# Kernel optimization log

Measured on AMD Instinct MI355X. Metric: run time of the kernel, lower is better.

The kernel has to match this reference:

```python
import jax, jax.numpy as jnp
import numpy as np

S, B, D, H = 2048, 2, 1024, 16
DK = D // H  # 64

def setup_inputs() -> dict:
    key0 = jax.random.key(0)
    ks = jax.random.split(key0, 11)
    scale = 0.02
    inp = {
        'query': jax.random.normal(ks[0], (S, B, D), jnp.float32),
        'key':   jax.random.normal(ks[1], (S, B, D), jnp.float32),
        'value': jax.random.normal(ks[2], (S, B, D), jnp.float32),
        # nn.Linear weights stored torch-style [out_features, in_features]
        'Wq': jax.random.normal(ks[3], (H * DK, D), jnp.float32) * scale,
        'bq': jnp.zeros((H * DK,), jnp.float32),
        'Wk': jax.random.normal(ks[4], (H * DK, D), jnp.float32) * scale,
        'bk': jnp.zeros((H * DK,), jnp.float32),
        'Wv': jax.random.normal(ks[5], (H * DK, D), jnp.float32) * scale,
        'bv': jnp.zeros((H * DK,), jnp.float32),
        'Wo': jax.random.normal(ks[6], (D, D), jnp.float32) * scale,
        'bo': jnp.zeros((D,), jnp.float32),
    }
    return inp

def _proj(x, W, b):
    # x: [S,B,D] -> [S,B,H,DK]
    y = jnp.einsum('sbd,ed->sbe', x, W) + b
    return y.reshape(x.shape[0], x.shape[1], H, DK)

def reference(query, key, value, Wq, bq, Wk, bk, Wv, bv, Wo, bo):
    q = _proj(query, Wq, bq)   # [S,B,H,DK]
    k = _proj(key,   Wk, bk)
    v = _proj(value, Wv, bv)
    # NOTE: original forward never applies self.scale -> unscaled QK^T (faithful)
    scores = jnp.einsum('ibhd,jbhd->ijbh', q, k)      # [Sq,Sk,B,H]
    attn = jax.nn.softmax(scores, axis=1)             # softmax over key axis j
    x = jnp.einsum('ijbh,jbhd->ibhd', attn, v)        # [S,B,H,DK]
    x = x.reshape(q.shape[0], q.shape[1], H * DK)     # [S,B,D]
    out = jnp.einsum('sbd,ed->sbe', x, Wo) + bo       # [S,B,D]
    return out
```

## Files before the change

### kernel.cpp

```cpp
#include <hip/hip_runtime.h>
#include <stdint.h>

#define S_LEN  2048
#define BATCH  2
#define DMODEL 1024
#define NHEAD  16
#define DKH    64

typedef __attribute__((ext_vector_type(8))) __bf16 bf16x8;
typedef __attribute__((ext_vector_type(4))) float  f32x4;
typedef unsigned short u16;
typedef unsigned int   u32;

#if __has_builtin(__builtin_amdgcn_exp2f)
#define EXP2(x) __builtin_amdgcn_exp2f(x)
#else
#define EXP2(x) __expf(0.69314718055994531f * (x))
#endif

#define SWAP32(a, b) asm("v_permlane32_swap_b32 %0, %1" : "+v"(a), "+v"(b))
#define SWAP16(a, b) asm("v_permlane16_swap_b32 %0, %1" : "+v"(a), "+v"(b))

__device__ __forceinline__ u16 f2bf(float f) {
  union { float f; u32 u; } v; v.f = f;
  u32 r = v.u + 0x7fffu + ((v.u >> 16) & 1u);
  return (u16)(r >> 16);
}

__global__ void cvt3_kernel(const float4* __restrict__ a, const float4* __restrict__ b,
                            const float4* __restrict__ c,
                            ushort4* __restrict__ oa, ushort4* __restrict__ ob,
                            ushort4* __restrict__ oc, int n4) {
  int i = blockIdx.x * blockDim.x + threadIdx.x;
  if (i >= n4) return;
  const float4* src = (blockIdx.y == 0) ? a : (blockIdx.y == 1) ? b : c;
  ushort4*      dst = (blockIdx.y == 0) ? oa : (blockIdx.y == 1) ? ob : oc;
  float4 v = src[i];
  ushort4 o;
  o.x = f2bf(v.x); o.y = f2bf(v.y); o.z = f2bf(v.z); o.w = f2bf(v.w);
  dst[i] = o;
}

__global__ void cvt4_kernel(const float4* __restrict__ a, const float4* __restrict__ b,
                            const float4* __restrict__ c, const float4* __restrict__ d,
                            ushort4* __restrict__ oa, ushort4* __restrict__ ob,
                            ushort4* __restrict__ oc, ushort4* __restrict__ od, int n4) {
  int i = blockIdx.x * blockDim.x + threadIdx.x;
  if (i >= n4) return;
  const float4* src = (blockIdx.y == 0) ? a : (blockIdx.y == 1) ? b : (blockIdx.y == 2) ? c : d;
  ushort4*      dst = (blockIdx.y == 0) ? oa : (blockIdx.y == 1) ? ob : (blockIdx.y == 2) ? oc : od;
  float4 v = src[i];
  ushort4 o;
  o.x = f2bf(v.x); o.y = f2bf(v.y); o.z = f2bf(v.z); o.w = f2bf(v.w);
  dst[i] = o;
}

__global__ __launch_bounds__(256, 2)
void gemm_qkv(const u16* __restrict__ Abase, const u16* __restrict__ Wbase,
              const float* __restrict__ b0, const float* __restrict__ b1,
              const float* __restrict__ b2, u16* __restrict__ Obase) {
  __shared__ __align__(16) u16 As[128 * 32];
  __shared__ __align__(16) u16 Bs[128 * 32];

  const int z = blockIdx.z;
  const u16* A = Abase + (size_t)z * (S_LEN * BATCH * DMODEL);
  const u16* W = Wbase + (size_t)z * (DMODEL * DMODEL);
  const float* bias = (z == 0) ? b0 : (z == 1) ? b1 : b2;
  u16* O = Obase + (size_t)z * (S_LEN * BATCH * DMODEL);
  const float scl = (z == 0) ? 1.4426950408889634f : 1.0f;

  const int tid  = threadIdx.x;
  const int wave = tid >> 6, lane = tid & 63;
  const int quad = lane >> 4, lcol = lane & 15;
  const int m0 = blockIdx.y * 128, n0 = blockIdx.x * 128;
  const int wm = (wave >> 1) * 64, wn = (wave & 1) * 64;

  f32x4 acc[4][4] = {};

  for (int k0 = 0; k0 < DMODEL; k0 += 32) {
#pragma unroll
    for (int r = 0; r < 2; ++r) {
      int idx = r * 256 + tid;
      int row = idx >> 2, col = (idx & 3) * 8;
      const u16* gA = A + (size_t)(m0 + row) * DMODEL + k0 + col;
      const u16* gW = W + (size_t)(n0 + row) * DMODEL + k0 + col;
      u16* lA = As + (size_t)(r * 256 + (tid & 192)) * 8;
      u16* lB = Bs + (size_t)(r * 256 + (tid & 192)) * 8;
      __builtin_amdgcn_global_load_lds((const __attribute__((address_space(1))) void*)gA,
                                       (__attribute__((address_space(3))) void*)lA, 16, 0, 0);
      __builtin_amdgcn_global_load_lds((const __attribute__((address_space(1))) void*)gW,
                                       (__attribute__((address_space(3))) void*)lB, 16, 0, 0);
    }
    __syncthreads();

    const u16* aBase = As + (wm + lcol) * 32 + quad * 8;
    const u16* bBase = Bs + (wn + lcol) * 32 + quad * 8;
    bf16x8 af[4], bfr[4];
#pragma unroll
    for (int i = 0; i < 4; ++i) af[i]  = *(const bf16x8*)(aBase + i * 16 * 32);
#pragma unroll
    for (int j = 0; j < 4; ++j) bfr[j] = *(const bf16x8*)(bBase + j * 16 * 32);
#pragma unroll
    for (int i = 0; i < 4; ++i)
#pragma unroll
      for (int j = 0; j < 4; ++j)
        acc[i][j] = __builtin_amdgcn_mfma_f32_16x16x32_bf16(af[i], bfr[j], acc[i][j], 0, 0, 0);
    __syncthreads();
  }

#pragma unroll
  for (int i = 0; i < 4; ++i) {
#pragma unroll
    for (int j = 0; j < 4; ++j) {
      int n = n0 + wn + j * 16 + lcol;
      int h = n >> 6, dk = n & 63;
      float bv = bias[n];
#pragma unroll
      for (int r = 0; r < 4; ++r) {
        int m = m0 + wm + i * 16 + quad * 4 + r;
        int s = m >> 1, b = m & 1;
        O[((size_t)(b * NHEAD + h) * S_LEN + s) * DKH + dk] = f2bf((acc[i][j][r] + bv) * scl);
      }
    }
  }
}

__global__ __launch_bounds__(256, 2)
void gemm_o(const u16* __restrict__ A, const u16* __restrict__ W,
            const float* __restrict__ bias, float* __restrict__ O) {
  __shared__ __align__(16) u16 As[128 * 32];
  __shared__ __align__(16) u16 Bs[64 * 32];

  const int tid  = threadIdx.x;
  const int wave = tid >> 6, lane = tid & 63;
  const int quad = lane >> 4, lcol = lane & 15;
  const int m0 = blockIdx.y * 128, n0 = blockIdx.x * 64;
  const int wm = (wave >> 1) * 64, wn = (wave & 1) * 32;

  f32x4 acc[4][2] = {};

  for (int k0 = 0; k0 < DMODEL; k0 += 32) {
#pragma unroll
    for (int r = 0; r < 2; ++r) {
      int idx = r * 256 + tid;
      int row = idx >> 2, col = (idx & 3) * 8;
      const u16* gA = A + (size_t)(m0 + row) * DMODEL + k0 + col;
      u16* lA = As + (size_t)(r * 256 + (tid & 192)) * 8;
      __builtin_amdgcn_global_load_lds((const __attribute__((address_space(1))) void*)gA,
                                       (__attribute__((address_space(3))) void*)lA, 16, 0, 0);
    }
    {
      int row = tid >> 2, col = (tid & 3) * 8;
      const u16* gW = W + (size_t)(n0 + row) * DMODEL + k0 + col;
      u16* lB = Bs + (size_t)(tid & 192) * 8;
      __builtin_amdgcn_global_load_lds((const __attribute__((address_space(1))) void*)gW,
                                       (__attribute__((address_space(3))) void*)lB, 16, 0, 0);
    }
    __syncthreads();

    const u16* aBase = As + (wm + lcol) * 32 + quad * 8;
    const u16* bBase = Bs + (wn + lcol) * 32 + quad * 8;
    bf16x8 af[4], bfr[2];
#pragma unroll
    for (int i = 0; i < 4; ++i) af[i]  = *(const bf16x8*)(aBase + i * 16 * 32);
#pragma unroll
    for (int j = 0; j < 2; ++j) bfr[j] = *(const bf16x8*)(bBase + j * 16 * 32);
#pragma unroll
    for (int i = 0; i < 4; ++i)
#pragma unroll
      for (int j = 0; j < 2; ++j)
        acc[i][j] = __builtin_amdgcn_mfma_f32_16x16x32_bf16(af[i], bfr[j], acc[i][j], 0, 0, 0);
    __syncthreads();
  }

#pragma unroll
  for (int i = 0; i < 4; ++i) {
#pragma unroll
    for (int j = 0; j < 2; ++j) {
      int n = n0 + wn + j * 16 + lcol;
      float bv = bias[n];
#pragma unroll
      for (int r = 0; r < 4; ++r) {
        int m = m0 + wm + i * 16 + quad * 4 + r;
        O[(size_t)m * DMODEL + n] = acc[i][j][r] + bv;
      }
    }
  }
}

__global__ __launch_bounds__(512, 4)
void attn_kernel(const u16* __restrict__ Q, const u16* __restrict__ K,
                 const u16* __restrict__ V, u16* __restrict__ O) {
  __shared__ __align__(16) u16 smem[2 * 4608 + 2 * 4608];
  __shared__ float l_s2[4][32];
  u16* Ks  = smem;
  u16* Vts = smem + 2 * 4608;

  const int tid  = threadIdx.x;
  const int wave = tid >> 6, lane = tid & 63;
  const int quad = lane >> 4, lcol = lane & 15;
  const int h  = wave >> 2;
  const int qw = wave & 3;
  const int bh = blockIdx.y;
  const int q0 = blockIdx.x * 128;

  const size_t headOff = (size_t)bh * S_LEN * DKH;
  const u16* Qg = Q + headOff;
  const u16* Kg = K + headOff;
  const u16* Vg = V + headOff;

  bf16x8 qf[2][2];
#pragma unroll
  for (int s = 0; s < 2; ++s)
#pragma unroll
    for (int ks = 0; ks < 2; ++ks)
      qf[s][ks] = *(const bf16x8*)(Qg + (size_t)(q0 + qw * 32 + s * 16 + lcol) * DKH +
                                   ks * 32 + quad * 8);

  const int krow  = tid >> 3, kch = tid & 7;
  const int vhalf = (lane >> 5), vkp = lane & 31;
  const int vo    = wave;

  uint4 kr0 = *(const uint4*)(Kg + (size_t)krow * DKH + kch * 8);
  uint4 kr1 = *(const uint4*)(Kg + (size_t)(S_LEN / 2 + krow) * DKH + kch * 8);
  uint4 vr0, vr1;
  {
    const u16* vp = Vg + (size_t)(vhalf * (S_LEN / 2) + 2 * vkp) * DKH + 8 * vo;
    vr0 = *(const uint4*)vp;
    vr1 = *(const uint4*)(vp + DKH);
  }

  f32x4 o_acc[2][4] = {};
  float lsum[2] = {0.f, 0.f};

  for (int it = 0; it < 16; ++it) {
    *(uint4*)(Ks + (size_t)krow * 72 + kch * 8)        = kr0;
    *(uint4*)(Ks + (size_t)(64 + krow) * 72 + kch * 8) = kr1;
    {
      u16* vd = Vts + vhalf * 4608;
#pragma unroll
      for (int jj = 0; jj < 4; ++jj) {
        u32 aw = ((const u32*)&vr0)[jj], bw = ((const u32*)&vr1)[jj];
        *(u32*)(vd + (size_t)(8 * vo + 2 * jj) * 72 + 2 * vkp)     = __builtin_amdgcn_perm(bw, aw, 0x05040100u);
        *(u32*)(vd + (size_t)(8 * vo + 2 * jj + 1) * 72 + 2 * vkp) = __builtin_amdgcn_perm(bw, aw, 0x07060302u);
      }
    }
    __syncthreads();

    if (it < 15) {
      int nb = (it + 1) * 64;
      kr0 = *(const uint4*)(Kg + (size_t)(nb + krow) * DKH + kch * 8);
      kr1 = *(const uint4*)(Kg + (size_t)(S_LEN / 2 + nb + krow) * DKH + kch * 8);
      const u16* vp = Vg + (size_t)(vhalf * (S_LEN / 2) + nb + 2 * vkp) * DKH + 8 * vo;
      vr0 = *(const uint4*)vp;
      vr1 = *(const uint4*)(vp + DKH);
    }

    const u16* kb = Ks  + h * 4608;
    const u16* vb = Vts + h * 4608;

    f32x4 sc[2][4] = {};
#pragma unroll
    for (int ks = 0; ks < 2; ++ks) {
      bf16x8 ak[4];
#pragma unroll
      for (int j = 0; j < 4; ++j)
        ak[j] = *(const bf16x8*)(kb + (j * 16 + lcol) * 72 + ks * 32 + quad * 8);
      __builtin_amdgcn_s_setprio(1);
#pragma unroll
      for (int s = 0; s < 2; ++s)
#pragma unroll
        for (int j = 0; j < 4; ++j)
          sc[s][j] = __builtin_amdgcn_mfma_f32_16x16x32_bf16(ak[j], qf[s][ks], sc[s][j], 0, 0, 0);
      __builtin_amdgcn_s_setprio(0);
    }

    bf16x8 pa[2][2];
#pragma unroll
    for (int s = 0; s < 2; ++s) {
      u32 ww[4][2];
#pragma unroll
      for (int j = 0; j < 4; ++j) {
        float p0 = EXP2(sc[s][j][0]);
        float p1 = EXP2(sc[s][j][1]);
        float p2 = EXP2(sc[s][j][2]);
        float p3 = EXP2(sc[s][j][3]);
        lsum[s] += (p0 + p1) + (p2 + p3);
        asm("v_cvt_pk_bf16_f32 %0, %1, %2" : "=v"(ww[j][0]) : "v"(p0), "v"(p1));
        asm("v_cvt_pk_bf16_f32 %0, %1, %2" : "=v"(ww[j][1]) : "v"(p2), "v"(p3));
      }
#pragma unroll
      for (int ks = 0; ks < 2; ++ks) {
        u32 a0 = ww[2 * ks][0], b0 = ww[2 * ks + 1][0];
        SWAP32(a0, b0); SWAP16(a0, b0);
        u32 a1 = ww[2 * ks][1], b1 = ww[2 * ks + 1][1];
        SWAP32(a1, b1); SWAP16(a1, b1);
        union { u32 u[4]; bf16x8 v; } f;
        f.u[0] = a0; f.u[1] = a1; f.u[2] = b0; f.u[3] = b1;
        pa[s][ks] = f.v;
      }
    }

#pragma unroll
    for (int ks = 0; ks < 2; ++ks) {
      bf16x8 bv[4];
#pragma unroll
      for (int jd = 0; jd < 4; ++jd)
        bv[jd] = *(const bf16x8*)(vb + (jd * 16 + lcol) * 72 + ks * 32 + quad * 8);
      __builtin_amdgcn_s_setprio(1);
#pragma unroll
      for (int s = 0; s < 2; ++s)
#pragma unroll
        for (int jd = 0; jd < 4; ++jd)
          o_acc[s][jd] = __builtin_amdgcn_mfma_f32_16x16x32_bf16(pa[s][ks], bv[jd], o_acc[s][jd], 0, 0, 0);
      __builtin_amdgcn_s_setprio(0);
    }

    __syncthreads();
  }

#pragma unroll
  for (int s = 0; s < 2; ++s) {
    lsum[s] += __shfl_xor(lsum[s], 16);
    lsum[s] += __shfl_xor(lsum[s], 32);
  }

  float* scr = (float*)smem;
  if (wave >= 4) {
    int base = ((wave - 4) * 64 + lane) * 36;
#pragma unroll
    for (int s = 0; s < 2; ++s)
#pragma unroll
      for (int jd = 0; jd < 4; ++jd)
        *(f32x4*)(scr + base + (s * 4 + jd) * 4) = o_acc[s][jd];
    if (lane < 16) {
      l_s2[wave - 4][lane]      = lsum[0];
      l_s2[wave - 4][16 + lane] = lsum[1];
    }
  }
  __syncthreads();
  if (wave < 4) {
    int base = (wave * 64 + lane) * 36;
#pragma unroll
    for (int s = 0; s < 2; ++s)
#pragma unroll
      for (int jd = 0; jd < 4; ++jd)
        o_acc[s][jd] += *(const f32x4*)(scr + base + (s * 4 + jd) * 4);
    float tot0 = lsum[0] + l_s2[wave][lcol];
    float tot1 = lsum[1] + l_s2[wave][16 + lcol];

    const int b = bh >> 4, hh = bh & 15;
#pragma unroll
    for (int s = 0; s < 2; ++s) {
      float tot = (s == 0) ? tot0 : tot1;
#pragma unroll
      for (int r = 0; r < 4; ++r) {
        float inv = 1.f / __shfl(tot, quad * 4 + r);
        int sq = q0 + wave * 32 + s * 16 + quad * 4 + r;
#pragma unroll
        for (int jd = 0; jd < 4; ++jd) {
          int dk = jd * 16 + lcol;
          O[((size_t)(sq * BATCH + b)) * DMODEL + hh * DKH + dk] = f2bf(o_acc[s][jd][r] * inv);
        }
      }
    }
  }
}

extern "C" void kernel_launch(void* const* d_in, const int* in_sizes, int n_in,
                              void* d_out, int out_size, void* d_ws, size_t ws_size,
                              hipStream_t stream) {
  const float* q  = (const float*)d_in[0];
  const float* k  = (const float*)d_in[1];
  const float* v  = (const float*)d_in[2];
  const float* Wq = (const float*)d_in[3];
  const float* bq = (const float*)d_in[4];
  const float* Wk = (const float*)d_in[5];
  const float* bk = (const float*)d_in[6];
  const float* Wv = (const float*)d_in[7];
  const float* bv = (const float*)d_in[8];
  const float* Wo = (const float*)d_in[9];
  const float* bo = (const float*)d_in[10];

  const int NX = S_LEN * BATCH * DMODEL;
  const int NW = DMODEL * DMODEL;

  u16* ws  = (u16*)d_ws;
  u16* Xq  = ws;
  u16* Wqb = Xq  + 3 * (size_t)NX;
  u16* Qb  = Wqb + 4 * (size_t)NW;
  u16* Xo  = Qb  + 3 * (size_t)NX;

  u16* Xk  = Xq + NX, *Xv = Xq + 2 * (size_t)NX;
  u16* Wkb = Wqb + NW, *Wvb = Wqb + 2 * (size_t)NW, *Wob = Wqb + 3 * (size_t)NW;
  u16* Kb  = Qb + NX, *Vb = Qb + 2 * (size_t)NX;

  dim3 g3(NX / 4 / 256, 3);
  cvt3_kernel<<<g3, 256, 0, stream>>>((const float4*)q, (const float4*)k, (const float4*)v,
                                      (ushort4*)Xq, (ushort4*)Xk, (ushort4*)Xv, NX / 4);
  dim3 g4(NW / 4 / 256, 4);
  cvt4_kernel<<<g4, 256, 0, stream>>>((const float4*)Wq, (const float4*)Wk, (const float4*)Wv,
                                      (const float4*)Wo,
                                      (ushort4*)Wqb, (ushort4*)Wkb, (ushort4*)Wvb, (ushort4*)Wob,
                                      NW / 4);

  dim3 gqkv(DMODEL / 128, (S_LEN * BATCH) / 128, 3);
  gemm_qkv<<<gqkv, 256, 0, stream>>>(Xq, Wqb, bq, bk, bv, Qb);

  dim3 ga(S_LEN / 128, BATCH * NHEAD);
  attn_kernel<<<ga, 512, 0, stream>>>(Qb, Kb, Vb, Xo);

  dim3 go(DMODEL / 64, (S_LEN * BATCH) / 128);
  gemm_o<<<go, 256, 0, stream>>>(Xo, Wob, bo, (float*)d_out);
}
```

Before: 228.0 us.

## Merge conversion kernels, swizzle blocks per XCD, and enlarge attention query tile

```diff
diff --git a/kernel.cpp b/kernel.cpp
--- a/kernel.cpp
+++ b/kernel.cpp
@@ -27,31 +27,28 @@
   return (u16)(r >> 16);
 }
 
-__global__ void cvt3_kernel(const float4* __restrict__ a, const float4* __restrict__ b,
-                            const float4* __restrict__ c,
-                            ushort4* __restrict__ oa, ushort4* __restrict__ ob,
-                            ushort4* __restrict__ oc, int n4) {
+__global__ void cvt_all(const float4* __restrict__ q, const float4* __restrict__ k,
+                        const float4* __restrict__ v,
+                        const float4* __restrict__ wq, const float4* __restrict__ wk,
+                        const float4* __restrict__ wv, const float4* __restrict__ wo,
+                        ushort4* __restrict__ dst) {
+  const int NX4 = (S_LEN * BATCH * DMODEL) / 4;
+  const int NW4 = (DMODEL * DMODEL) / 4;
   int i = blockIdx.x * blockDim.x + threadIdx.x;
-  if (i >= n4) return;
-  const float4* src = (blockIdx.y == 0) ? a : (blockIdx.y == 1) ? b : c;
-  ushort4*      dst = (blockIdx.y == 0) ? oa : (blockIdx.y == 1) ? ob : oc;
-  float4 v = src[i];
+  const float4* src;
+  int off;
+  if (i < 3 * NX4) {
+    src = (i < NX4) ? q : (i < 2 * NX4) ? k : v;
+    off = i & (NX4 - 1);
+  } else {
+    int j = i - 3 * NX4;
+    int t = j >> 18;
+    src = (t == 0) ? wq : (t == 1) ? wk : (t == 2) ? wv : wo;
+    off = j & (NW4 - 1);
+  }
+  float4 val = src[off];
   ushort4 o;
-  o.x = f2bf(v.x); o.y = f2bf(v.y); o.z = f2bf(v.z); o.w = f2bf(v.w);
-  dst[i] = o;
-}
-
-__global__ void cvt4_kernel(const float4* __restrict__ a, const float4* __restrict__ b,
-                            const float4* __restrict__ c, const float4* __restrict__ d,
-                            ushort4* __restrict__ oa, ushort4* __restrict__ ob,
-                            ushort4* __restrict__ oc, ushort4* __restrict__ od, int n4) {
-  int i = blockIdx.x * blockDim.x + threadIdx.x;
-  if (i >= n4) return;
-  const float4* src = (blockIdx.y == 0) ? a : (blockIdx.y == 1) ? b : (blockIdx.y == 2) ? c : d;
-  ushort4*      dst = (blockIdx.y == 0) ? oa : (blockIdx.y == 1) ? ob : (blockIdx.y == 2) ? oc : od;
-  float4 v = src[i];
-  ushort4 o;
-  o.x = f2bf(v.x); o.y = f2bf(v.y); o.z = f2bf(v.z); o.w = f2bf(v.w);
+  o.x = f2bf(val.x); o.y = f2bf(val.y); o.z = f2bf(val.z); o.w = f2bf(val.w);
   dst[i] = o;
 }
 
@@ -62,7 +59,12 @@
   __shared__ __align__(16) u16 As[128 * 32];
   __shared__ __align__(16) u16 Bs[128 * 32];
 
-  const int z = blockIdx.z;
+  const int L = blockIdx.x + (blockIdx.y << 3) + (blockIdx.z << 8);
+  const int xcd = L & 7, sl = L >> 3;
+  const int z  = sl >> 5;
+  const int y  = xcd * 4 + ((sl >> 3) & 3);
+  const int nx = sl & 7;
+
   const u16* A = Abase + (size_t)z * (S_LEN * BATCH * DMODEL);
   const u16* W = Wbase + (size_t)z * (DMODEL * DMODEL);
   const float* bias = (z == 0) ? b0 : (z == 1) ? b1 : b2;
@@ -72,7 +74,7 @@
   const int tid  = threadIdx.x;
   const int wave = tid >> 6, lane = tid & 63;
   const int quad = lane >> 4, lcol = lane & 15;
-  const int m0 = blockIdx.y * 128, n0 = blockIdx.x * 128;
+  const int m0 = y * 128, n0 = nx * 128;
   const int wm = (wave >> 1) * 64, wn = (wave & 1) * 64;
 
   f32x4 acc[4][4] = {};
@@ -131,10 +133,15 @@
   __shared__ __align__(16) u16 As[128 * 32];
   __shared__ __align__(16) u16 Bs[64 * 32];
 
+  const int L = blockIdx.x + (blockIdx.y << 4);
+  const int xcd = L & 7, sl = L >> 3;
+  const int y = xcd * 4 + (sl >> 4);
+  const int x = sl & 15;
+
   const int tid  = threadIdx.x;
   const int wave = tid >> 6, lane = tid & 63;
   const int quad = lane >> 4, lcol = lane & 15;
-  const int m0 = blockIdx.y * 128, n0 = blockIdx.x * 64;
+  const int m0 = y * 128, n0 = x * 64;
   const int wm = (wave >> 1) * 64, wn = (wave & 1) * 32;
 
   f32x4 acc[4][2] = {};
@@ -188,37 +195,40 @@
   }
 }
 
-__global__ __launch_bounds__(512, 4)
+__global__ __launch_bounds__(512, 2)
 void attn_kernel(const u16* __restrict__ Q, const u16* __restrict__ K,
                  const u16* __restrict__ V, u16* __restrict__ O) {
-  __shared__ __align__(16) u16 smem[2 * 4608 + 2 * 4608];
-  __shared__ float l_s2[4][32];
+  __shared__ __align__(16) u16 smem[9216 + 9216];
+  __shared__ float ls2[4][4][16];
   u16* Ks  = smem;
-  u16* Vts = smem + 2 * 4608;
+  u16* Vts = smem + 9216;
 
   const int tid  = threadIdx.x;
   const int wave = tid >> 6, lane = tid & 63;
   const int quad = lane >> 4, lcol = lane & 15;
-  const int h  = wave >> 2;
-  const int qw = wave & 3;
-  const int bh = blockIdx.y;
-  const int q0 = blockIdx.x * 128;
+  const int qg = wave & 3;
+  const int kh = wave >> 2;
+
+  const int L = blockIdx.x + (blockIdx.y << 3);
+  const int xcd = L & 7, slot = L >> 3;
+  const int bh = xcd * 4 + (slot >> 3);
+  const int q0 = (slot & 7) * 256;
 
   const size_t headOff = (size_t)bh * S_LEN * DKH;
   const u16* Qg = Q + headOff;
   const u16* Kg = K + headOff;
   const u16* Vg = V + headOff;
 
-  bf16x8 qf[2][2];
-#pragma unroll
-  for (int s = 0; s < 2; ++s)
-#pragma unroll
-    for (int ks = 0; ks < 2; ++ks)
-      qf[s][ks] = *(const bf16x8*)(Qg + (size_t)(q0 + qw * 32 + s * 16 + lcol) * DKH +
-                                   ks * 32 + quad * 8);
+  bf16x8 qf[4][2];
+#pragma unroll
+  for (int s = 0; s < 4; ++s)
+#pragma unroll
+    for (int kc = 0; kc < 2; ++kc)
+      qf[s][kc] = *(const bf16x8*)(Qg + (size_t)(q0 + qg * 64 + s * 16 + lcol) * DKH +
+                                   kc * 32 + quad * 8);
 
   const int krow  = tid >> 3, kch = tid & 7;
-  const int vhalf = (lane >> 5), vkp = lane & 31;
+  const int vhalf = lane >> 5, vkp = lane & 31;
   const int vo    = wave;
 
   uint4 kr0 = *(const uint4*)(Kg + (size_t)krow * DKH + kch * 8);
@@ -230,8 +240,8 @@
     vr1 = *(const uint4*)(vp + DKH);
   }
 
-  f32x4 o_acc[2][4] = {};
-  float lsum[2] = {0.f, 0.f};
+  f32x4 o_acc[4][4] = {};
+  float lsum[4] = {0.f, 0.f, 0.f, 0.f};
 
   for (int it = 0; it < 16; ++it) {
     *(uint4*)(Ks + (size_t)krow * 72 + kch * 8)        = kr0;
@@ -256,63 +266,61 @@
       vr1 = *(const uint4*)(vp + DKH);
     }
 
-    const u16* kb = Ks  + h * 4608;
-    const u16* vb = Vts + h * 4608;
-
-    f32x4 sc[2][4] = {};
-#pragma unroll
-    for (int ks = 0; ks < 2; ++ks) {
-      bf16x8 ak[4];
-#pragma unroll
-      for (int j = 0; j < 4; ++j)
-        ak[j] = *(const bf16x8*)(kb + (j * 16 + lcol) * 72 + ks * 32 + quad * 8);
+    const u16* kb = Ks  + kh * 64 * 72;
+    const u16* vb = Vts + kh * 4608;
+
+#pragma unroll
+    for (int g = 0; g < 2; ++g) {
+      bf16x8 ak[2][2];
+#pragma unroll
+      for (int jb = 0; jb < 2; ++jb)
+#pragma unroll
+        for (int kc = 0; kc < 2; ++kc)
+          ak[jb][kc] = *(const bf16x8*)(kb + (g * 32 + jb * 16 + lcol) * 72 + kc * 32 + quad * 8);
+      f32x4 sc[2][4] = {};
       __builtin_amdgcn_s_setprio(1);
 #pragma unroll
-      for (int s = 0; s < 2; ++s)
-#pragma unroll
-        for (int j = 0; j < 4; ++j)
-          sc[s][j] = __builtin_amdgcn_mfma_f32_16x16x32_bf16(ak[j], qf[s][ks], sc[s][j], 0, 0, 0);
+      for (int kc = 0; kc < 2; ++kc)
+#pragma unroll
+        for (int jb = 0; jb < 2; ++jb)
+#pragma unroll
+          for (int s = 0; s < 4; ++s)
+            sc[jb][s] = __builtin_amdgcn_mfma_f32_16x16x32_bf16(ak[jb][kc], qf[s][kc], sc[jb][s], 0, 0, 0);
       __builtin_amdgcn_s_setprio(0);
-    }
-
-    bf16x8 pa[2][2];
-#pragma unroll
-    for (int s = 0; s < 2; ++s) {
-      u32 ww[4][2];
-#pragma unroll
-      for (int j = 0; j < 4; ++j) {
-        float p0 = EXP2(sc[s][j][0]);
-        float p1 = EXP2(sc[s][j][1]);
-        float p2 = EXP2(sc[s][j][2]);
-        float p3 = EXP2(sc[s][j][3]);
-        lsum[s] += (p0 + p1) + (p2 + p3);
-        asm("v_cvt_pk_bf16_f32 %0, %1, %2" : "=v"(ww[j][0]) : "v"(p0), "v"(p1));
-        asm("v_cvt_pk_bf16_f32 %0, %1, %2" : "=v"(ww[j][1]) : "v"(p2), "v"(p3));
-      }
-#pragma unroll
-      for (int ks = 0; ks < 2; ++ks) {
-        u32 a0 = ww[2 * ks][0], b0 = ww[2 * ks + 1][0];
+
+      bf16x8 pa[4];
+#pragma unroll
+      for (int s = 0; s < 4; ++s) {
+        u32 ww[2][2];
+#pragma unroll
+        for (int jb = 0; jb < 2; ++jb) {
+          float p0 = EXP2(sc[jb][s][0]);
+          float p1 = EXP2(sc[jb][s][1]);
+          float p2 = EXP2(sc[jb][s][2]);
+          float p3 = EXP2(sc[jb][s][3]);
+          lsum[s] += (p0 + p1) + (p2 + p3);
+          asm("v_cvt_pk_bf16_f32 %0, %1, %2" : "=v"(ww[jb][0]) : "v"(p0), "v"(p1));
+          asm("v_cvt_pk_bf16_f32 %0, %1, %2" : "=v"(ww[jb][1]) : "v"(p2), "v"(p3));
+        }
+        u32 a0 = ww[0][0], b0 = ww[1][0];
         SWAP32(a0, b0); SWAP16(a0, b0);
-        u32 a1 = ww[2 * ks][1], b1 = ww[2 * ks + 1][1];
+        u32 a1 = ww[0][1], b1 = ww[1][1];
         SWAP32(a1, b1); SWAP16(a1, b1);
         union { u32 u[4]; bf16x8 v; } f;
         f.u[0] = a0; f.u[1] = a1; f.u[2] = b0; f.u[3] = b1;
-        pa[s][ks] = f.v;
+        pa[s] = f.v;
       }
-    }
-
-#pragma unroll
-    for (int ks = 0; ks < 2; ++ks) {
+
       bf16x8 bv[4];
 #pragma unroll
       for (int jd = 0; jd < 4; ++jd)
-        bv[jd] = *(const bf16x8*)(vb + (jd * 16 + lcol) * 72 + ks * 32 + quad * 8);
+        bv[jd] = *(const bf16x8*)(vb + (jd * 16 + lcol) * 72 + g * 32 + quad * 8);
       __builtin_amdgcn_s_setprio(1);
 #pragma unroll
-      for (int s = 0; s < 2; ++s)
+      for (int s = 0; s < 4; ++s)
 #pragma unroll
         for (int jd = 0; jd < 4; ++jd)
-          o_acc[s][jd] = __builtin_amdgcn_mfma_f32_16x16x32_bf16(pa[s][ks], bv[jd], o_acc[s][jd], 0, 0, 0);
+          o_acc[s][jd] = __builtin_amdgcn_mfma_f32_16x16x32_bf16(pa[s], bv[jd], o_acc[s][jd], 0, 0, 0);
       __builtin_amdgcn_s_setprio(0);
     }
 
@@ -320,43 +328,59 @@
   }
 
 #pragma unroll
-  for (int s = 0; s < 2; ++s) {
+  for (int s = 0; s < 4; ++s) {
     lsum[s] += __shfl_xor(lsum[s], 16);
     lsum[s] += __shfl_xor(lsum[s], 32);
   }
 
   float* scr = (float*)smem;
-  if (wave >= 4) {
-    int base = ((wave - 4) * 64 + lane) * 36;
+  const int cbase = (qg * 64 + lane) * 32;
+  if (kh == 1) {
 #pragma unroll
     for (int s = 0; s < 2; ++s)
 #pragma unroll
       for (int jd = 0; jd < 4; ++jd)
-        *(f32x4*)(scr + base + (s * 4 + jd) * 4) = o_acc[s][jd];
+        *(f32x4*)(scr + cbase + (s * 4 + jd) * 4) = o_acc[s][jd];
     if (lane < 16) {
-      l_s2[wave - 4][lane]      = lsum[0];
-      l_s2[wave - 4][16 + lane] = lsum[1];
+#pragma unroll
+      for (int s = 0; s < 4; ++s) ls2[qg][s][lane] = lsum[s];
     }
   }
   __syncthreads();
-  if (wave < 4) {
-    int base = (wave * 64 + lane) * 36;
+  if (kh == 0) {
 #pragma unroll
     for (int s = 0; s < 2; ++s)
 #pragma unroll
       for (int jd = 0; jd < 4; ++jd)
-        o_acc[s][jd] += *(const f32x4*)(scr + base + (s * 4 + jd) * 4);
-    float tot0 = lsum[0] + l_s2[wave][lcol];
-    float tot1 = lsum[1] + l_s2[wave][16 + lcol];
+        o_acc[s][jd] += *(const f32x4*)(scr + cbase + (s * 4 + jd) * 4);
+  }
+  __syncthreads();
+  if (kh == 1) {
+#pragma unroll
+    for (int s = 2; s < 4; ++s)
+#pragma unroll
+      for (int jd = 0; jd < 4; ++jd)
+        *(f32x4*)(scr + cbase + ((s - 2) * 4 + jd) * 4) = o_acc[s][jd];
+  }
+  __syncthreads();
+  if (kh == 0) {
+#pragma unroll
+    for (int s = 2; s < 4; ++s)
+#pragma unroll
+      for (int jd = 0; jd < 4; ++jd)
+        o_acc[s][jd] += *(const f32x4*)(scr + cbase + ((s - 2) * 4 + jd) * 4);
+
+    float tot[4];
+#pragma unroll
+    for (int s = 0; s < 4; ++s) tot[s] = lsum[s] + ls2[qg][s][lcol];
 
     const int b = bh >> 4, hh = bh & 15;
 #pragma unroll
-    for (int s = 0; s < 2; ++s) {
-      float tot = (s == 0) ? tot0 : tot1;
+    for (int s = 0; s < 4; ++s) {
 #pragma unroll
       for (int r = 0; r < 4; ++r) {
-        float inv = 1.f / __shfl(tot, quad * 4 + r);
-        int sq = q0 + wave * 32 + s * 16 + quad * 4 + r;
+        float inv = 1.f / __shfl(tot[s], quad * 4 + r);
+        int sq = q0 + qg * 64 + s * 16 + quad * 4 + r;
 #pragma unroll
         for (int jd = 0; jd < 4; ++jd) {
           int dk = jd * 16 + lcol;
@@ -391,23 +415,18 @@
   u16* Qb  = Wqb + 4 * (size_t)NW;
   u16* Xo  = Qb  + 3 * (size_t)NX;
 
-  u16* Xk  = Xq + NX, *Xv = Xq + 2 * (size_t)NX;
-  u16* Wkb = Wqb + NW, *Wvb = Wqb + 2 * (size_t)NW, *Wob = Wqb + 3 * (size_t)NW;
+  u16* Wob = Wqb + 3 * (size_t)NW;
   u16* Kb  = Qb + NX, *Vb = Qb + 2 * (size_t)NX;
 
-  dim3 g3(NX / 4 / 256, 3);
-  cvt3_kernel<<<g3, 256, 0, stream>>>((const float4*)q, (const float4*)k, (const float4*)v,
-                                      (ushort4*)Xq, (ushort4*)Xk, (ushort4*)Xv, NX / 4);
-  dim3 g4(NW / 4 / 256, 4);
-  cvt4_kernel<<<g4, 256, 0, stream>>>((const float4*)Wq, (const float4*)Wk, (const float4*)Wv,
-                                      (const float4*)Wo,
-                                      (ushort4*)Wqb, (ushort4*)Wkb, (ushort4*)Wvb, (ushort4*)Wob,
-                                      NW / 4);
+  const int n4 = (3 * NX + 4 * NW) / 4;
+  cvt_all<<<n4 / 256, 256, 0, stream>>>((const float4*)q, (const float4*)k, (const float4*)v,
+                                        (const float4*)Wq, (const float4*)Wk, (const float4*)Wv,
+                                        (const float4*)Wo, (ushort4*)ws);
 
   dim3 gqkv(DMODEL / 128, (S_LEN * BATCH) / 128, 3);
   gemm_qkv<<<gqkv, 256, 0, stream>>>(Xq, Wqb, bq, bk, bv, Qb);
 
-  dim3 ga(S_LEN / 128, BATCH * NHEAD);
+  dim3 ga(S_LEN / 256, BATCH * NHEAD);
   attn_kernel<<<ga, 512, 0, stream>>>(Qb, Kb, Vb, Xo);
 
   dim3 go(DMODEL / 64, (S_LEN * BATCH) / 128);
```

Result: faster. 214.3 us (-6.0%).
